# Performance work log

Hardware: AMD Instinct MI355X
Metric: run time of the kernel (lower is better)

## Reference

```python
import jax, jax.numpy as jnp
import numpy as np

N = 50000        # nodes
E = 600000       # edges (before self-loops)
VOCAB = 100000
EMB = 128
HID = 128
G = 64           # graphs in batch
NEG_SLOPE = 0.2


def setup_inputs() -> dict:
    key = jax.random.key(0)
    ks = jax.random.split(key, 16)
    x_idx = jax.random.randint(ks[0], (N,), 0, VOCAB)
    edge_index = jax.random.randint(ks[1], (2, E), 0, N)
    edge_attr = jax.random.uniform(ks[2], (E,), dtype=jnp.float32)
    batch = jnp.sort(jax.random.randint(ks[3], (N,), 0, G))
    # embedding table; padding_idx=0 row zeroed as in nn.Embedding(padding_idx=0)
    emb_table = (jax.random.normal(ks[4], (VOCAB, EMB), dtype=jnp.float32) * 0.05).at[0].set(0.0)
    glorot = lambda k, shp: jax.random.normal(k, shp, dtype=jnp.float32) * np.float32(np.sqrt(2.0 / sum(shp)))
    W1 = glorot(ks[5], (HID, EMB))
    att_src1 = glorot(ks[6], (HID,)) * 0.0 + jax.random.normal(ks[6], (HID,), dtype=jnp.float32) * np.float32(np.sqrt(2.0 / (HID + 1)))
    att_dst1 = jax.random.normal(ks[7], (HID,), dtype=jnp.float32) * np.float32(np.sqrt(2.0 / (HID + 1)))
    W2 = glorot(ks[8], (HID, HID))
    att_src2 = jax.random.normal(ks[9], (HID,), dtype=jnp.float32) * np.float32(np.sqrt(2.0 / (HID + 1)))
    att_dst2 = jax.random.normal(ks[10], (HID,), dtype=jnp.float32) * np.float32(np.sqrt(2.0 / (HID + 1)))
    W3 = glorot(ks[11], (HID // 2, HID))
    b3 = jnp.zeros((HID // 2,), jnp.float32)
    W4 = glorot(ks[12], (2, HID // 2))
    b4 = jnp.zeros((2,), jnp.float32)
    return {"x_idx": x_idx, "edge_index": edge_index, "edge_attr": edge_attr, "batch": batch,
            "emb_table": emb_table, "W1": W1, "att_src1": att_src1, "att_dst1": att_dst1,
            "W2": W2, "att_src2": att_src2, "att_dst2": att_dst2,
            "W3": W3, "b3": b3, "W4": W4, "b4": b4}


def _segment_softmax(logits, seg, n):
    m = jax.ops.segment_max(logits, seg, num_segments=n)
    e = jnp.exp(logits - m[seg])
    s = jax.ops.segment_sum(e, seg, num_segments=n)
    return e / (s[seg] + 1e-16)


def _edge_attr_gat_conv(x, src, dst, ea, W, a_src, a_dst, n):
    H = x @ W.T                                   # [n, out]
    # per-edge score: (H_i . a_dst) + (H_j . a_src); compute per-node then gather
    alpha = (H @ a_dst)[dst] + (H @ a_src)[src]   # [e]
    alpha = jnp.where(alpha >= 0, alpha, NEG_SLOPE * alpha)
    alpha = alpha * ea                            # multiplicative edge attr
    alpha = _segment_softmax(alpha, dst, n)       # softmax over in-neighborhoods
    return jax.ops.segment_sum(H[src] * alpha[:, None], dst, num_segments=n)


def reference(x_idx, edge_index, edge_attr, batch, emb_table,
              W1, att_src1, att_dst1, W2, att_src2, att_dst2, W3, b3, W4, b4):
    n = x_idx.shape[0]
    loops = jnp.arange(n)
    # add_self_loops (done inside each conv in torch; same edges both layers)
    src = jnp.concatenate([edge_index[0], loops])
    dst = jnp.concatenate([edge_index[1], loops])  # edge_index_i (aggregation index)
    ea = jnp.concatenate([edge_attr, jnp.ones((n,), edge_attr.dtype)])
    x = emb_table[x_idx]
    x = jax.nn.relu(_edge_attr_gat_conv(x, src, dst, ea, W1, att_src1, att_dst1, n))
    x = jax.nn.relu(_edge_attr_gat_conv(x, src, dst, ea, W2, att_src2, att_dst2, n))
    # global_mean_pool
    sums = jax.ops.segment_sum(x, batch, num_segments=G)
    counts = jax.ops.segment_sum(jnp.ones((n,), x.dtype), batch, num_segments=G)
    g = sums / jnp.maximum(counts, 1.0)[:, None]
    # MLP head (dropout = identity at eval)
    h = jax.nn.relu(g @ W3.T + b3)
    return h @ W4.T + b4
```

## Files before the change

kernel.cpp:

```cpp
#include <hip/hip_runtime.h>
#include <cstdint>
#include <cstddef>


__device__ __forceinline__ float wave_sum(float v) {
#pragma unroll
  for (int m = 32; m >= 1; m >>= 1) v += __shfl_xor(v, m, 64);
  return v;
}


__global__ void init_kernel(int* __restrict__ deg, float* __restrict__ gsum,
                            int* __restrict__ gstart, int* __restrict__ gend,
                            int N, int G) {
  int i = blockIdx.x * blockDim.x + threadIdx.x;
  if (i < N) deg[i] = 1;
  if (i < G * 128) gsum[i] = 0.f;
  if (i < G) { gstart[i] = 0; gend[i] = 0; }
}

__global__ void count_deg_kernel(const int* __restrict__ edge_index,
                                 int* __restrict__ deg, int E) {
  int e = blockIdx.x * blockDim.x + threadIdx.x;
  if (e < E) atomicAdd(&deg[edge_index[E + e]], 1);
}

__global__ void scan1_kernel(const int* __restrict__ deg, int* __restrict__ bsum, int N) {
  __shared__ int ws[4];
  int tid = threadIdx.x;
  int i = blockIdx.x * 256 + tid;
  int v = (i < N) ? deg[i] : 0;
#pragma unroll
  for (int m = 32; m >= 1; m >>= 1) v += __shfl_xor(v, m, 64);
  if ((tid & 63) == 0) ws[tid >> 6] = v;
  __syncthreads();
  if (tid == 0) bsum[blockIdx.x] = ws[0] + ws[1] + ws[2] + ws[3];
}

__device__ __forceinline__ int block_excl_scan_256(int v, int tid, int* wsum) {
  int lane = tid & 63, wid = tid >> 6;
  int incl = v;
#pragma unroll
  for (int off = 1; off < 64; off <<= 1) {
    int t = __shfl_up(incl, off, 64);
    if (lane >= off) incl += t;
  }
  if (lane == 63) wsum[wid] = incl;
  __syncthreads();
  int woff = 0;
#pragma unroll
  for (int w = 0; w < 4; ++w)
    if (w < wid) woff += wsum[w];
  return woff + incl - v;
}

__global__ void scan2_kernel(const int* __restrict__ bsum, int* __restrict__ boff,
                             int* __restrict__ row_ptr, int nb, int N) {
  __shared__ int wsum[4];
  int tid = threadIdx.x;
  int v = (tid < nb) ? bsum[tid] : 0;
  int excl = block_excl_scan_256(v, tid, wsum);
  if (tid < nb) boff[tid] = excl;
  if (tid == 255) row_ptr[N] = excl + v;
}

__global__ void scan3_fill_kernel(const int* __restrict__ deg, const int* __restrict__ boff,
                                  int* __restrict__ row_ptr, int2* __restrict__ pk,
                                  int* __restrict__ cur, int N) {
  __shared__ int wsum[4];
  int tid = threadIdx.x;
  int i = blockIdx.x * 256 + tid;
  int v = (i < N) ? deg[i] : 0;
  int excl = block_excl_scan_256(v, tid, wsum);
  if (i < N) {
    int p = boff[blockIdx.x] + excl;
    row_ptr[i] = p;
    pk[p] = make_int2(i, __float_as_int(1.0f));
    cur[i] = p + 1;
  }
}

__global__ void fillB_kernel(const int* __restrict__ edge_index, const float* __restrict__ ea,
                             int* __restrict__ cur, int2* __restrict__ pk, int E) {
  int e = blockIdx.x * blockDim.x + threadIdx.x;
  if (e < E) {
    int d0 = edge_index[E + e];
    int s0 = edge_index[e];
    float a0 = ea[e];
    int p = atomicAdd(&cur[d0], 1);
    pk[p] = make_int2(s0, __float_as_int(a0));
  }
}


__global__ __launch_bounds__(256) void gemm_att_kernel(
    const float* __restrict__ Xin, const int* __restrict__ gidx,
    const float* __restrict__ W,
    const float* __restrict__ a_src, const float* __restrict__ a_dst,
    float* __restrict__ H, float* __restrict__ sv, float* __restrict__ dv, int N) {
  __shared__ float XsT[32][64];
  __shared__ float Wt[32][128];
  __shared__ float av[2][128];

  int tid = threadIdx.x;
  int tx = tid & 15, ty = tid >> 4;
  int rb = blockIdx.x * 64;

  if (tid < 128) { av[0][tid] = a_src[tid]; av[1][tid] = a_dst[tid]; }

  int r0 = tid & 63;
  int q0 = tid >> 6;
  int gr0 = rb + r0; if (gr0 >= N) gr0 = N - 1;
  const float* rp0 = gidx ? (Xin + (size_t)gidx[gr0] * 128) : (Xin + (size_t)gr0 * 128);

  float acc[4][8];
#pragma unroll
  for (int r = 0; r < 4; ++r)
#pragma unroll
    for (int j = 0; j < 8; ++j) acc[r][j] = 0.f;

#pragma unroll
  for (int ks = 0; ks < 4; ++ks) {
    const int k0 = ks * 32;
    __syncthreads();
    {
      float4 v0 = *(const float4*)(rp0 + k0 + q0 * 4);
      float4 v1 = *(const float4*)(rp0 + k0 + (q0 + 4) * 4);
      XsT[q0 * 4 + 0][r0] = v0.x; XsT[q0 * 4 + 1][r0] = v0.y;
      XsT[q0 * 4 + 2][r0] = v0.z; XsT[q0 * 4 + 3][r0] = v0.w;
      XsT[(q0 + 4) * 4 + 0][r0] = v1.x; XsT[(q0 + 4) * 4 + 1][r0] = v1.y;
      XsT[(q0 + 4) * 4 + 2][r0] = v1.z; XsT[(q0 + 4) * 4 + 3][r0] = v1.w;
    }
#pragma unroll
    for (int it = 0; it < 4; ++it) {
      int idx = tid + it * 256;
      int c = idx & 127, q = idx >> 7;
      float4 v = *(const float4*)(W + (size_t)c * 128 + k0 + q * 4);
      Wt[q * 4 + 0][c] = v.x; Wt[q * 4 + 1][c] = v.y;
      Wt[q * 4 + 2][c] = v.z; Wt[q * 4 + 3][c] = v.w;
    }
    __syncthreads();
#pragma unroll 8
    for (int k = 0; k < 32; ++k) {
      float4 xa = *(const float4*)&XsT[k][ty * 4];
      float4 wl = *(const float4*)&Wt[k][tx * 4];
      float4 wh = *(const float4*)&Wt[k][tx * 4 + 64];
      float xr[4] = {xa.x, xa.y, xa.z, xa.w};
      float wv[8] = {wl.x, wl.y, wl.z, wl.w, wh.x, wh.y, wh.z, wh.w};
#pragma unroll
      for (int r = 0; r < 4; ++r)
#pragma unroll
        for (int j = 0; j < 8; ++j) acc[r][j] = fmaf(xr[r], wv[j], acc[r][j]);
    }
  }

#pragma unroll
  for (int r = 0; r < 4; ++r) {
    int gr = rb + ty * 4 + r;
    float ps = 0.f, pd = 0.f;
#pragma unroll
    for (int j = 0; j < 4; ++j) {
      ps = fmaf(acc[r][j], av[0][tx * 4 + j], ps);
      ps = fmaf(acc[r][4 + j], av[0][tx * 4 + 64 + j], ps);
      pd = fmaf(acc[r][j], av[1][tx * 4 + j], pd);
      pd = fmaf(acc[r][4 + j], av[1][tx * 4 + 64 + j], pd);
    }
#pragma unroll
    for (int m = 1; m < 16; m <<= 1) {
      ps += __shfl_xor(ps, m, 64);
      pd += __shfl_xor(pd, m, 64);
    }
    if (gr < N) {
      float4 lo = make_float4(acc[r][0], acc[r][1], acc[r][2], acc[r][3]);
      float4 hi = make_float4(acc[r][4], acc[r][5], acc[r][6], acc[r][7]);
      *(float4*)(H + (size_t)gr * 128 + tx * 4) = lo;
      *(float4*)(H + (size_t)gr * 128 + 64 + tx * 4) = hi;
      if (tx == 0) { sv[gr] = ps; dv[gr] = pd; }
    }
  }
}


__global__ __launch_bounds__(256) void agg_kernel(
    const float* __restrict__ H, const float* __restrict__ sv, const float* __restrict__ dv,
    const int* __restrict__ row_ptr, const int2* __restrict__ pk,
    float* __restrict__ Xout, int N) {
  int tid = threadIdx.x;
  int hw = tid >> 5;
  int cl = tid & 31;
  int node = blockIdx.x * 8 + hw;
  if (node >= N) return;
  int p0 = row_ptr[node], p1 = row_ptr[node + 1];
  int deg = p1 - p0;
  float di = dv[node];

  float4 acc = make_float4(0.f, 0.f, 0.f, 0.f);
  float S = 0.f;

  if (deg <= 32) {
    float f = -3.4e38f; int sE = 0;
    if (cl < deg) {
      int2 pe = pk[p0 + cl];
      sE = pe.x;
      float t = di + sv[sE];
      t = (t >= 0.f) ? t : 0.2f * t;
      f = t * __int_as_float(pe.y);
    }
    float m = f;
#pragma unroll
    for (int s = 16; s >= 1; s >>= 1) m = fmaxf(m, __shfl_xor(m, s, 32));
    float w = (cl < deg) ? expf(f - m) : 0.f;
    float Ss = w;
#pragma unroll
    for (int s = 16; s >= 1; s >>= 1) Ss += __shfl_xor(Ss, s, 32);
    S = Ss;
    for (int t0 = 0; t0 < deg; t0 += 4) {
      float4 v[4]; float wv[4];
#pragma unroll
      for (int u = 0; u < 4; ++u) {
        int idx = t0 + u;
        float wj = __shfl(w, idx, 32);
        int sj = __shfl(sE, idx, 32);
        bool valid = idx < deg;
        wv[u] = valid ? wj : 0.f;
        const float4* hr = (const float4*)(H + (size_t)(valid ? sj : 0) * 128);
        v[u] = hr[cl];
      }
#pragma unroll
      for (int u = 0; u < 4; ++u) {
        acc.x = fmaf(wv[u], v[u].x, acc.x);
        acc.y = fmaf(wv[u], v[u].y, acc.y);
        acc.z = fmaf(wv[u], v[u].z, acc.z);
        acc.w = fmaf(wv[u], v[u].w, acc.w);
      }
    }
  } else {
    float m = -3.4e38f;
    for (int p = p0; p < p1; p += 32) {
      int e = p + cl;
      float f = -3.4e38f;
      if (e < p1) {
        int2 pe = pk[e];
        float t = di + sv[pe.x];
        t = (t >= 0.f) ? t : 0.2f * t;
        f = t * __int_as_float(pe.y);
      }
#pragma unroll
      for (int s = 16; s >= 1; s >>= 1) f = fmaxf(f, __shfl_xor(f, s, 32));
      m = fmaxf(m, f);
    }
    for (int p = p0; p < p1; p += 32) {
      int cnt = min(32, p1 - p);
      float w = 0.f; int sE = 0;
      if (cl < cnt) {
        int2 pe = pk[p + cl];
        sE = pe.x;
        float t = di + sv[sE];
        t = (t >= 0.f) ? t : 0.2f * t;
        w = expf(t * __int_as_float(pe.y) - m);
      }
      float Ss = w;
#pragma unroll
      for (int s = 16; s >= 1; s >>= 1) Ss += __shfl_xor(Ss, s, 32);
      S += Ss;
      for (int t0 = 0; t0 < cnt; t0 += 4) {
        float4 v[4]; float wv[4];
#pragma unroll
        for (int u = 0; u < 4; ++u) {
          int idx = t0 + u;
          float wj = __shfl(w, idx, 32);
          int sj = __shfl(sE, idx, 32);
          bool valid = idx < cnt;
          wv[u] = valid ? wj : 0.f;
          const float4* hr = (const float4*)(H + (size_t)(valid ? sj : 0) * 128);
          v[u] = hr[cl];
        }
#pragma unroll
        for (int u = 0; u < 4; ++u) {
          acc.x = fmaf(wv[u], v[u].x, acc.x);
          acc.y = fmaf(wv[u], v[u].y, acc.y);
          acc.z = fmaf(wv[u], v[u].z, acc.z);
          acc.w = fmaf(wv[u], v[u].w, acc.w);
        }
      }
    }
  }

  float sc = 1.0f / (S + 1e-16f);
  float4 o;
  o.x = fmaxf(acc.x * sc, 0.f);
  o.y = fmaxf(acc.y * sc, 0.f);
  o.z = fmaxf(acc.z * sc, 0.f);
  o.w = fmaxf(acc.w * sc, 0.f);
  *(float4*)(Xout + (size_t)node * 128 + cl * 4) = o;
}


__global__ void batch_bounds_kernel(const int* __restrict__ batch,
                                    int* __restrict__ gstart, int* __restrict__ gend, int N) {
  int i = blockIdx.x * blockDim.x + threadIdx.x;
  if (i >= N) return;
  int b = batch[i];
  if (i == 0 || batch[i - 1] != b) gstart[b] = i;
  if (i == N - 1 || batch[i + 1] != b) gend[b] = i + 1;
}

__global__ void pool_kernel(const float* __restrict__ X, const int* __restrict__ batch,
                            float* __restrict__ gsum, int N) {
  int col = threadIdx.x & 127;
  int half = threadIdx.x >> 7;
  int base = blockIdx.x * 128;
  int cur = -1; float acc = 0.f;
  for (int j = half; j < 128; j += 2) {
    int n = base + j;
    if (n >= N) break;
    int g = batch[n];
    if (g != cur) {
      if (cur >= 0) atomicAdd(&gsum[cur * 128 + col], acc);
      cur = g; acc = 0.f;
    }
    acc += X[(size_t)n * 128 + col];
  }
  if (cur >= 0) atomicAdd(&gsum[cur * 128 + col], acc);
}

__global__ __launch_bounds__(256) void head_kernel(
    const float* __restrict__ gsum,
    const int* __restrict__ gstart, const int* __restrict__ gend,
    const float* __restrict__ W3, const float* __restrict__ b3,
    const float* __restrict__ W4, const float* __restrict__ b4,
    float* __restrict__ out, int G) {
  __shared__ float gv[128];
  __shared__ float h[64];
  int gid = blockIdx.x;
  int tid = threadIdx.x;
  float cnt = (float)(gend[gid] - gstart[gid]);
  if (cnt < 1.f) cnt = 1.f;
  if (tid < 128) gv[tid] = gsum[(size_t)gid * 128 + tid] / cnt;
  __syncthreads();
  {
    int c = tid >> 2, part = tid & 3;
    const float4* w = (const float4*)(W3 + (size_t)c * 128 + part * 32);
    const float4* gg = (const float4*)(gv + part * 32);
    float acc = 0.f;
#pragma unroll
    for (int k = 0; k < 8; ++k) {
      float4 a = gg[k], b = w[k];
      acc = fmaf(a.x, b.x, acc); acc = fmaf(a.y, b.y, acc);
      acc = fmaf(a.z, b.z, acc); acc = fmaf(a.w, b.w, acc);
    }
    acc += __shfl_xor(acc, 1, 64);
    acc += __shfl_xor(acc, 2, 64);
    if (part == 0) { float v = acc + b3[c]; h[c] = (v > 0.f) ? v : 0.f; }
  }
  __syncthreads();
  if (tid < 128) {
    int o = tid >> 6, k = tid & 63;
    float p = h[k] * W4[o * 64 + k];
    p = wave_sum(p);
    if (k == 0) out[gid * 2 + o] = p + b4[o];
  }
}


extern "C" void kernel_launch(void* const* d_in, const int* in_sizes, int n_in,
                              void* d_out, int out_size, void* d_ws, size_t ws_size,
                              hipStream_t stream) {
  const int* x_idx = (const int*)d_in[0];
  const int* edge_index = (const int*)d_in[1];
  const float* edge_attr = (const float*)d_in[2];
  const int* batch = (const int*)d_in[3];
  const float* emb = (const float*)d_in[4];
  const float* W1 = (const float*)d_in[5];
  const float* as1 = (const float*)d_in[6];
  const float* ad1 = (const float*)d_in[7];
  const float* W2 = (const float*)d_in[8];
  const float* as2 = (const float*)d_in[9];
  const float* ad2 = (const float*)d_in[10];
  const float* W3 = (const float*)d_in[11];
  const float* b3 = (const float*)d_in[12];
  const float* W4 = (const float*)d_in[13];
  const float* b4 = (const float*)d_in[14];

  const int N = in_sizes[0];
  const int E = in_sizes[2];
  const int G = out_size / 2;
  const int ET = E + N;

  uint8_t* wp = (uint8_t*)d_ws;
  auto take = [&](size_t bytes) -> void* {
    void* p = (void*)wp;
    wp += (bytes + 255) & ~(size_t)255;
    return p;
  };
  float* H    = (float*)take((size_t)N * 128 * 4);
  float* X    = (float*)take((size_t)N * 128 * 4);
  float* sv   = (float*)take((size_t)N * 4);
  float* dv   = (float*)take((size_t)N * 4);
  int*   deg  = (int*)take((size_t)N * 4);
  int*   rowp = (int*)take((size_t)(N + 1) * 4);
  int*   cur  = (int*)take((size_t)N * 4);
  int*   bsum = (int*)take(256 * 4);
  int*   boff = (int*)take(256 * 4);
  int2*  pk   = (int2*)take((size_t)ET * 8);
  float* gsum = (float*)take((size_t)G * 128 * 4);
  int*   gstart = (int*)take((size_t)G * 4);
  int*   gend   = (int*)take((size_t)G * 4);
  (void)ws_size; (void)n_in;

  const int nb = (N + 255) / 256;
  const int eb = (E + 255) / 256;

  init_kernel<<<nb, 256, 0, stream>>>(deg, gsum, gstart, gend, N, G);
  count_deg_kernel<<<eb, 256, 0, stream>>>(edge_index, deg, E);
  scan1_kernel<<<nb, 256, 0, stream>>>(deg, bsum, N);
  scan2_kernel<<<1, 256, 0, stream>>>(bsum, boff, rowp, nb, N);
  scan3_fill_kernel<<<nb, 256, 0, stream>>>(deg, boff, rowp, pk, cur, N);
  fillB_kernel<<<eb, 256, 0, stream>>>(edge_index, edge_attr, cur, pk, E);

  const int gb = (N + 63) / 64;
  const int ab = (N + 7) / 8;
  gemm_att_kernel<<<gb, 256, 0, stream>>>(emb, x_idx, W1, as1, ad1, H, sv, dv, N);
  agg_kernel<<<ab, 256, 0, stream>>>(H, sv, dv, rowp, pk, X, N);
  gemm_att_kernel<<<gb, 256, 0, stream>>>(X, nullptr, W2, as2, ad2, H, sv, dv, N);
  agg_kernel<<<ab, 256, 0, stream>>>(H, sv, dv, rowp, pk, X, N);
  batch_bounds_kernel<<<nb, 256, 0, stream>>>(batch, gstart, gend, N);
  pool_kernel<<<(N + 127) / 128, 256, 0, stream>>>(X, batch, gsum, N);
  head_kernel<<<G, 256, 0, stream>>>(gsum, gstart, gend, W3, b3, W4, b4, (float*)d_out, G);
}
```

Baseline: 276.6 us.

## Split GAT aggregation into two feature-half passes with cached edge weights

```diff
diff --git a/kernel.cpp b/kernel.cpp
--- a/kernel.cpp
+++ b/kernel.cpp
@@ -181,9 +181,10 @@
 }
 
 
-__global__ __launch_bounds__(256) void agg_kernel(
+__global__ __launch_bounds__(256) void agg_pass1_kernel(
     const float* __restrict__ H, const float* __restrict__ sv, const float* __restrict__ dv,
     const int* __restrict__ row_ptr, const int2* __restrict__ pk,
+    int2* __restrict__ pw, float* __restrict__ invS,
     float* __restrict__ Xout, int N) {
   int tid = threadIdx.x;
   int hw = tid >> 5;
@@ -194,7 +195,7 @@
   int deg = p1 - p0;
   float di = dv[node];
 
-  float4 acc = make_float4(0.f, 0.f, 0.f, 0.f);
+  float2 acc = make_float2(0.f, 0.f);
   float S = 0.f;
 
   if (deg <= 32) {
@@ -214,8 +215,9 @@
 #pragma unroll
     for (int s = 16; s >= 1; s >>= 1) Ss += __shfl_xor(Ss, s, 32);
     S = Ss;
+    if (cl < deg) pw[p0 + cl] = make_int2(sE, __float_as_int(w));
     for (int t0 = 0; t0 < deg; t0 += 4) {
-      float4 v[4]; float wv[4];
+      float2 v[4]; float wv[4];
 #pragma unroll
       for (int u = 0; u < 4; ++u) {
         int idx = t0 + u;
@@ -223,15 +225,13 @@
         int sj = __shfl(sE, idx, 32);
         bool valid = idx < deg;
         wv[u] = valid ? wj : 0.f;
-        const float4* hr = (const float4*)(H + (size_t)(valid ? sj : 0) * 128);
+        const float2* hr = (const float2*)(H + (size_t)(valid ? sj : 0) * 128);
         v[u] = hr[cl];
       }
 #pragma unroll
       for (int u = 0; u < 4; ++u) {
         acc.x = fmaf(wv[u], v[u].x, acc.x);
         acc.y = fmaf(wv[u], v[u].y, acc.y);
-        acc.z = fmaf(wv[u], v[u].z, acc.z);
-        acc.w = fmaf(wv[u], v[u].w, acc.w);
       }
     }
   } else {
@@ -258,13 +258,14 @@
         float t = di + sv[sE];
         t = (t >= 0.f) ? t : 0.2f * t;
         w = expf(t * __int_as_float(pe.y) - m);
+        pw[p + cl] = make_int2(sE, __float_as_int(w));
       }
       float Ss = w;
 #pragma unroll
       for (int s = 16; s >= 1; s >>= 1) Ss += __shfl_xor(Ss, s, 32);
       S += Ss;
       for (int t0 = 0; t0 < cnt; t0 += 4) {
-        float4 v[4]; float wv[4];
+        float2 v[4]; float wv[4];
 #pragma unroll
         for (int u = 0; u < 4; ++u) {
           int idx = t0 + u;
@@ -272,27 +273,72 @@
           int sj = __shfl(sE, idx, 32);
           bool valid = idx < cnt;
           wv[u] = valid ? wj : 0.f;
-          const float4* hr = (const float4*)(H + (size_t)(valid ? sj : 0) * 128);
+          const float2* hr = (const float2*)(H + (size_t)(valid ? sj : 0) * 128);
           v[u] = hr[cl];
         }
 #pragma unroll
         for (int u = 0; u < 4; ++u) {
           acc.x = fmaf(wv[u], v[u].x, acc.x);
           acc.y = fmaf(wv[u], v[u].y, acc.y);
-          acc.z = fmaf(wv[u], v[u].z, acc.z);
-          acc.w = fmaf(wv[u], v[u].w, acc.w);
         }
       }
     }
   }
 
   float sc = 1.0f / (S + 1e-16f);
-  float4 o;
+  if (cl == 0) invS[node] = sc;
+  float2 o;
   o.x = fmaxf(acc.x * sc, 0.f);
   o.y = fmaxf(acc.y * sc, 0.f);
-  o.z = fmaxf(acc.z * sc, 0.f);
-  o.w = fmaxf(acc.w * sc, 0.f);
-  *(float4*)(Xout + (size_t)node * 128 + cl * 4) = o;
+  *(float2*)(Xout + (size_t)node * 128 + cl * 2) = o;
+}
+
+__global__ __launch_bounds__(256) void agg_pass2_kernel(
+    const float* __restrict__ H, const int* __restrict__ row_ptr,
+    const int2* __restrict__ pw, const float* __restrict__ invS,
+    float* __restrict__ Xout, int N) {
+  int tid = threadIdx.x;
+  int hw = tid >> 5;
+  int cl = tid & 31;
+  int node = blockIdx.x * 8 + hw;
+  if (node >= N) return;
+  int p0 = row_ptr[node], p1 = row_ptr[node + 1];
+
+  float2 acc = make_float2(0.f, 0.f);
+
+  for (int p = p0; p < p1; p += 32) {
+    int cnt = min(32, p1 - p);
+    float w = 0.f; int sE = 0;
+    if (cl < cnt) {
+      int2 pe = pw[p + cl];
+      sE = pe.x;
+      w = __int_as_float(pe.y);
+    }
+    for (int t0 = 0; t0 < cnt; t0 += 4) {
+      float2 v[4]; float wv[4];
+#pragma unroll
+      for (int u = 0; u < 4; ++u) {
+        int idx = t0 + u;
+        float wj = __shfl(w, idx, 32);
+        int sj = __shfl(sE, idx, 32);
+        bool valid = idx < cnt;
+        wv[u] = valid ? wj : 0.f;
+        const float2* hr = (const float2*)(H + (size_t)(valid ? sj : 0) * 128 + 64);
+        v[u] = hr[cl];
+      }
+#pragma unroll
+      for (int u = 0; u < 4; ++u) {
+        acc.x = fmaf(wv[u], v[u].x, acc.x);
+        acc.y = fmaf(wv[u], v[u].y, acc.y);
+      }
+    }
+  }
+
+  float sc = invS[node];
+  float2 o;
+  o.x = fmaxf(acc.x * sc, 0.f);
+  o.y = fmaxf(acc.y * sc, 0.f);
+  *(float2*)(Xout + (size_t)node * 128 + 64 + cl * 2) = o;
 }
 
 
@@ -403,6 +449,8 @@
   int*   bsum = (int*)take(256 * 4);
   int*   boff = (int*)take(256 * 4);
   int2*  pk   = (int2*)take((size_t)ET * 8);
+  int2*  pw   = (int2*)take((size_t)ET * 8);
+  float* invS = (float*)take((size_t)N * 4);
   float* gsum = (float*)take((size_t)G * 128 * 4);
   int*   gstart = (int*)take((size_t)G * 4);
   int*   gend   = (int*)take((size_t)G * 4);
@@ -421,9 +469,11 @@
   const int gb = (N + 63) / 64;
   const int ab = (N + 7) / 8;
   gemm_att_kernel<<<gb, 256, 0, stream>>>(emb, x_idx, W1, as1, ad1, H, sv, dv, N);
-  agg_kernel<<<ab, 256, 0, stream>>>(H, sv, dv, rowp, pk, X, N);
+  agg_pass1_kernel<<<ab, 256, 0, stream>>>(H, sv, dv, rowp, pk, pw, invS, X, N);
+  agg_pass2_kernel<<<ab, 256, 0, stream>>>(H, rowp, pw, invS, X, N);
   gemm_att_kernel<<<gb, 256, 0, stream>>>(X, nullptr, W2, as2, ad2, H, sv, dv, N);
-  agg_kernel<<<ab, 256, 0, stream>>>(H, sv, dv, rowp, pk, X, N);
+  agg_pass1_kernel<<<ab, 256, 0, stream>>>(H, sv, dv, rowp, pk, pw, invS, X, N);
+  agg_pass2_kernel<<<ab, 256, 0, stream>>>(H, rowp, pw, invS, X, N);
   batch_bounds_kernel<<<nb, 256, 0, stream>>>(batch, gstart, gend, N);
   pool_kernel<<<(N + 127) / 128, 256, 0, stream>>>(X, batch, gsum, N);
   head_kernel<<<G, 256, 0, stream>>>(gsum, gstart, gend, W3, b3, W4, b4, (float*)d_out, G);
```

Result: slower. 284.8 us (+3.0%).

## Partition CSR degree count and fill atomics by destination range per XCD

Applied to the files above, without the earlier changes.

```diff
diff --git a/kernel.cpp b/kernel.cpp
--- a/kernel.cpp
+++ b/kernel.cpp
@@ -2,6 +2,9 @@
 #include <cstdint>
 #include <cstddef>
 
+
+#define CSR_CHUNK 8192
+#define NXCD 8
 
 __device__ __forceinline__ float wave_sum(float v) {
 #pragma unroll
@@ -19,10 +22,16 @@
   if (i < G) { gstart[i] = 0; gend[i] = 0; }
 }
 
-__global__ void count_deg_kernel(const int* __restrict__ edge_index,
-                                 int* __restrict__ deg, int E) {
-  int e = blockIdx.x * blockDim.x + threadIdx.x;
-  if (e < E) atomicAdd(&deg[edge_index[E + e]], 1);
+__global__ void count_deg_part_kernel(const int* __restrict__ edge_index,
+                                      int* __restrict__ deg, int E, int RN) {
+  int r = blockIdx.x & (NXCD - 1);
+  int s = blockIdx.x >> 3;
+  int lo = r * RN, hi = lo + RN;
+  int e1 = min(E, (s + 1) * CSR_CHUNK);
+  for (int e = s * CSR_CHUNK + threadIdx.x; e < e1; e += blockDim.x) {
+    int d = edge_index[E + e];
+    if (d >= lo && d < hi) atomicAdd(&deg[d], 1);
+  }
 }
 
 __global__ void scan1_kernel(const int* __restrict__ deg, int* __restrict__ bsum, int N) {
@@ -80,15 +89,22 @@
   }
 }
 
-__global__ void fillB_kernel(const int* __restrict__ edge_index, const float* __restrict__ ea,
-                             int* __restrict__ cur, int2* __restrict__ pk, int E) {
-  int e = blockIdx.x * blockDim.x + threadIdx.x;
-  if (e < E) {
-    int d0 = edge_index[E + e];
-    int s0 = edge_index[e];
-    float a0 = ea[e];
-    int p = atomicAdd(&cur[d0], 1);
-    pk[p] = make_int2(s0, __float_as_int(a0));
+__global__ void fillB_part_kernel(const int* __restrict__ edge_index,
+                                  const float* __restrict__ ea,
+                                  int* __restrict__ cur, int2* __restrict__ pk,
+                                  int E, int RN) {
+  int r = blockIdx.x & (NXCD - 1);
+  int s = blockIdx.x >> 3;
+  int lo = r * RN, hi = lo + RN;
+  int e1 = min(E, (s + 1) * CSR_CHUNK);
+  for (int e = s * CSR_CHUNK + threadIdx.x; e < e1; e += blockDim.x) {
+    int d = edge_index[E + e];
+    if (d >= lo && d < hi) {
+      int s0 = edge_index[e];
+      float a0 = ea[e];
+      int p = atomicAdd(&cur[d], 1);
+      pk[p] = make_int2(s0, __float_as_int(a0));
+    }
   }
 }
 
@@ -409,14 +425,16 @@
   (void)ws_size; (void)n_in;
 
   const int nb = (N + 255) / 256;
-  const int eb = (E + 255) / 256;
+  const int RN = (N + NXCD - 1) / NXCD;
+  const int ns = (E + CSR_CHUNK - 1) / CSR_CHUNK;
+  const int pb = ns * NXCD;
 
   init_kernel<<<nb, 256, 0, stream>>>(deg, gsum, gstart, gend, N, G);
-  count_deg_kernel<<<eb, 256, 0, stream>>>(edge_index, deg, E);
+  count_deg_part_kernel<<<pb, 256, 0, stream>>>(edge_index, deg, E, RN);
   scan1_kernel<<<nb, 256, 0, stream>>>(deg, bsum, N);
   scan2_kernel<<<1, 256, 0, stream>>>(bsum, boff, rowp, nb, N);
   scan3_fill_kernel<<<nb, 256, 0, stream>>>(deg, boff, rowp, pk, cur, N);
-  fillB_kernel<<<eb, 256, 0, stream>>>(edge_index, edge_attr, cur, pk, E);
+  fillB_part_kernel<<<pb, 256, 0, stream>>>(edge_index, edge_attr, cur, pk, E, RN);
 
   const int gb = (N + 63) / 64;
   const int ab = (N + 7) / 8;
```

New measurement: 273.1 us. About the same (-1.2%).
